# Performance work log

Measured on AMD Instinct MI355X. Metric: run time of the kernel, lower is better.

Reference implementation:

```python
import jax, jax.numpy as jnp
import numpy as np

A, B = 0.0, 1.0
U_LEFT, U_RIGHT = 0.0, 0.0
BOUNDARY_PENALTY = 10.0
N_POINTS = 32768
K_TEST = 1024  # sine test functions
LAYERS = [1, 256, 256, 256, 1]


def setup_inputs() -> dict:
    key = jax.random.key(0)
    ks = jax.random.split(key, 2 + len(LAYERS) - 1)
    # Gauss-Lobatto-like nodes: sorted points in (A, B)
    x = jnp.sort(jax.random.uniform(ks[0], (N_POINTS, 1), dtype=jnp.float32,
                                    minval=A, maxval=B), axis=0)
    # positive quadrature weights, scaled so sum(weights) ~ (B - A)
    weights = jax.random.uniform(ks[1], (N_POINTS,), dtype=jnp.float32) * (2.0 * (B - A) / N_POINTS)
    inp = {"x": x, "weights": weights}
    for i in range(len(LAYERS) - 1):
        fin, fout = LAYERS[i], LAYERS[i + 1]
        inp[f"W{i}"] = jax.random.normal(ks[2 + i], (fin, fout), dtype=jnp.float32) / np.sqrt(fin).astype(np.float32)
        inp[f"b{i}"] = jnp.zeros((fout,), dtype=jnp.float32)
    return inp


def _mlp(h, params):
    # tanh MLP, no activation on the last layer (matches MLP.forward)
    n = len(params)
    for i, (W, b) in enumerate(params):
        h = h @ W + b
        if i < n - 1:
            h = jnp.tanh(h)
    return h


def reference(x, weights, W0, b0, W1, b1, W2, b2, W3, b3):
    params = [(W0, b0), (W1, b1), (W2, b2), (W3, b3)]
    xf = x[:, 0]                                   # [N]

    u = _mlp(x, params)                            # [N, 1]

    # u_xx at every quadrature node via grad-of-grad, vmapped over points
    def u_scalar(xv):
        return _mlp(xv.reshape(1, 1), params)[0, 0]
    u_xx = jax.vmap(jax.grad(jax.grad(u_scalar)))(xf)   # [N]

    # analytic sine test functions v_k(x) = sin(pi k x), k = 1..K
    k = jnp.arange(1, K_TEST + 1, dtype=x.dtype)        # [K]
    test = jnp.sin(jnp.pi * k[:, None] * xf[None, :])   # [K, N]

    source = jnp.sin(jnp.pi * xf)                       # f(x) on the grid, [N]

    # batched quadrature: one matvec replaces the per-k Integrate loop
    Fk = test @ (weights * source)                      # [K]
    Rk = -(test @ (weights * u_xx))                     # [K]  (method 1: -int u_xx v_k)

    loss_interior = jnp.mean((Rk - Fk) ** 2)
    loss_boundary = 0.5 * BOUNDARY_PENALTY * (
        (u[0, 0] - U_LEFT) ** 2 + (u[-1, 0] - U_RIGHT) ** 2
    )
    return jnp.stack([loss_interior, loss_boundary])
```

## Files before the change

kernel.cpp:

```cpp
#include <hip/hip_runtime.h>
#include <cmath>

#define N_PTS 32768
#define HID   256
#define KTEST 1024
#define MB    32
#define RS    264
#define SKC   256
#define SKYB  (N_PTS / SKC)
#define SKGRID (4 * SKYB)

typedef float  f32x4  __attribute__((ext_vector_type(4)));
typedef short  s16x8  __attribute__((ext_vector_type(8)));
typedef __bf16 bf16x8 __attribute__((ext_vector_type(8)));

__device__ __forceinline__ float b2f(unsigned short s) {
    return __uint_as_float(((unsigned int)s) << 16);
}
__device__ __forceinline__ unsigned short cvt16(float x) {
    return __builtin_bit_cast(unsigned short, (__bf16)x);
}
__device__ __forceinline__ void split2(float x, unsigned short& hi, unsigned short& lo) {
    unsigned int b = __float_as_uint(x);
    hi = (unsigned short)(b >> 16);
    float hf = __uint_as_float(b & 0xFFFF0000u);
    lo = cvt16(x - hf);
}
__device__ __forceinline__ float fast_tanh(float z) {
    float e = __expf(2.0f * z);
    return 1.0f - 2.0f / (e + 1.0f);
}

__global__ __launch_bounds__(64) void wswz_kernel(
    const float* __restrict__ W1, const float* __restrict__ W2,
    unsigned short* __restrict__ Wh1, unsigned short* __restrict__ Wl1,
    unsigned short* __restrict__ Wh2, unsigned short* __restrict__ Wl2,
    unsigned int* __restrict__ counter)
{
    const int lane = threadIdx.x;
    const int t  = blockIdx.x;
    const int kc = blockIdx.y;
    const float* W = blockIdx.z ? W2 : W1;
    unsigned short* Wh = blockIdx.z ? Wh2 : Wh1;
    unsigned short* Wl = blockIdx.z ? Wl2 : Wl1;
    const int q = lane >> 4, ln = lane & 15;
    const int n = t * 16 + ln;
    const int kbase = kc * 32 + q * 8;

    s16x8 hv, lv;
    #pragma unroll
    for (int j = 0; j < 8; ++j) {
        unsigned short h, l;
        split2(W[(kbase + j) * HID + n], h, l);
        hv[j] = (short)h; lv[j] = (short)l;
    }
    const int out = ((t * 8 + kc) * 64 + lane) * 8;
    *(s16x8*)(Wh + out) = hv;
    *(s16x8*)(Wl + out) = lv;

    if (lane == 0 && t == 0 && kc == 0 && blockIdx.z == 0)
        *counter = 0u;
}

__global__ __launch_bounds__(512, 4) void mlp_kernel(
    const float* __restrict__ x, const float* __restrict__ wq,
    const float* __restrict__ W0, const float* __restrict__ b0,
    const float* __restrict__ b1v, const float* __restrict__ b2v,
    const float* __restrict__ W3, const float* __restrict__ b3,
    const unsigned short* __restrict__ W1h, const unsigned short* __restrict__ W1l,
    const unsigned short* __restrict__ W2h, const unsigned short* __restrict__ W2l,
    float* __restrict__ u_arr, float* __restrict__ d_arr)
{
    __shared__ __align__(16) unsigned short Hb[3][MB][RS];

    const int tid = threadIdx.x;
    const int gp0 = blockIdx.x * MB;

    {
        const int m = tid & 31, jseg = tid >> 5;
        const float xm = x[gp0 + m];
        #pragma unroll 4
        for (int jj = 0; jj < 16; ++jj) {
            int j = jseg * 16 + jj;
            float w = W0[j];
            float z = fmaf(xm, w, b0[j]);
            float y = fast_tanh(z);
            float s = 1.0f - y * y;
            float yp = s * w;
            float ypp = -2.0f * y * yp * w;
            Hb[0][m][j] = cvt16(y);
            Hb[1][m][j] = cvt16(yp);
            Hb[2][m][j] = cvt16(ypp);
        }
    }
    __syncthreads();

    const int lane = tid & 63, wv = tid >> 6;
    const int q = lane >> 4, ln = lane & 15;

    const int fragbase = (wv * 2) * 8 * 512 + lane * 8;

    for (int layer = 0; layer < 2; ++layer) {
        const unsigned short* __restrict__ WhW = (layer ? W2h : W1h) + fragbase;
        const unsigned short* __restrict__ WlW = (layer ? W2l : W1l) + fragbase;
        const float* __restrict__ bb = layer ? b2v : b1v;

        f32x4 acc[3][2][2];
        #pragma unroll
        for (int s = 0; s < 3; ++s)
            #pragma unroll
            for (int mf = 0; mf < 2; ++mf)
                #pragma unroll
                for (int nt = 0; nt < 2; ++nt)
                    acc[s][mf][nt] = (f32x4){0.f, 0.f, 0.f, 0.f};

        s16x8 bh[2][2], bl[2][2];
        #pragma unroll
        for (int nt = 0; nt < 2; ++nt) {
            bh[0][nt] = *(const s16x8*)(WhW + nt * 4096);
            bl[0][nt] = *(const s16x8*)(WlW + nt * 4096);
        }

        int cur = 0;
        for (int kc = 0; kc < 8; ++kc) {
            const int nxt = cur ^ 1;
            if (kc < 7) {
                #pragma unroll
                for (int nt = 0; nt < 2; ++nt) {
                    const int off = nt * 4096 + (kc + 1) * 512;
                    bh[nxt][nt] = *(const s16x8*)(WhW + off);
                    bl[nxt][nt] = *(const s16x8*)(WlW + off);
                }
            }
            s16x8 av[3][2];
            #pragma unroll
            for (int s = 0; s < 3; ++s)
                #pragma unroll
                for (int mf = 0; mf < 2; ++mf)
                    av[s][mf] = *(const s16x8*)&Hb[s][mf * 16 + ln][kc * 32 + q * 8];
            #pragma unroll
            for (int s = 0; s < 3; ++s)
                #pragma unroll
                for (int mf = 0; mf < 2; ++mf)
                    #pragma unroll
                    for (int nt = 0; nt < 2; ++nt) {
                        acc[s][mf][nt] = __builtin_amdgcn_mfma_f32_16x16x32_bf16(
                            __builtin_bit_cast(bf16x8, av[s][mf]),
                            __builtin_bit_cast(bf16x8, bh[cur][nt]), acc[s][mf][nt], 0, 0, 0);
                        acc[s][mf][nt] = __builtin_amdgcn_mfma_f32_16x16x32_bf16(
                            __builtin_bit_cast(bf16x8, av[s][mf]),
                            __builtin_bit_cast(bf16x8, bl[cur][nt]), acc[s][mf][nt], 0, 0, 0);
                    }
            cur = nxt;
        }
        __syncthreads();

        #pragma unroll
        for (int nt = 0; nt < 2; ++nt) {
            const int c = wv * 32 + nt * 16 + ln;
            const float bias = bb[c];
            #pragma unroll
            for (int mf = 0; mf < 2; ++mf) {
                #pragma unroll
                for (int i = 0; i < 4; ++i) {
                    const int r = mf * 16 + q * 4 + i;
                    float z   = acc[0][mf][nt][i] + bias;
                    float zp  = acc[1][mf][nt][i];
                    float zpp = acc[2][mf][nt][i];
                    float y  = fast_tanh(z);
                    float s  = 1.0f - y * y;
                    float yp = s * zp;
                    float ypp = fmaf(s, zpp, -2.0f * y * yp * zp);
                    Hb[0][r][c] = cvt16(y);
                    if (layer == 0) Hb[1][r][c] = cvt16(yp);
                    Hb[2][r][c] = cvt16(ypp);
                }
            }
        }
        __syncthreads();
    }

    float* psum = (float*)&Hb[1][0][0];
    {
        const int m = tid & 31, seg = tid >> 5;
        float su = 0.f, sx = 0.f;
        #pragma unroll 4
        for (int jj = 0; jj < 16; ++jj) {
            int j = seg * 16 + jj;
            float w3 = W3[j];
            su = fmaf(b2f(Hb[0][m][j]), w3, su);
            sx = fmaf(b2f(Hb[2][m][j]), w3, sx);
        }
        psum[(0 * 16 + seg) * 32 + m] = su;
        psum[(1 * 16 + seg) * 32 + m] = sx;
    }
    __syncthreads();
    if (tid < MB) {
        float u = b3[0], uxx = 0.f;
        #pragma unroll
        for (int s2 = 0; s2 < 16; ++s2) {
            u   += psum[s2 * 32 + tid];
            uxx += psum[(16 + s2) * 32 + tid];
        }
        const int gp = gp0 + tid;
        u_arr[gp] = u;
        float xv = x[gp];
        d_arr[gp] = -wq[gp] * (uxx + sinpif(xv));
    }
}

__global__ __launch_bounds__(256) void sk_loss_kernel(
    const float* __restrict__ x, const float* __restrict__ d_arr,
    const float* __restrict__ u_arr, float* __restrict__ part,
    unsigned int* __restrict__ counter, float* __restrict__ out)
{
    __shared__ float xs_h[SKC], xs_l[SKC], ds[SKC];
    __shared__ float red[4];
    __shared__ int lastFlag;

    const int tid = threadIdx.x;
    const int k = blockIdx.x * 256 + tid;
    const int i0 = blockIdx.y * SKC;

    {
        float xv = x[i0 + tid];
        float xh = __uint_as_float(__float_as_uint(xv) & 0xFFFFF000u);
        xs_h[tid] = xh * 0.5f;
        xs_l[tid] = (xv - xh) * 0.5f;
        ds[tid]   = d_arr[i0 + tid];
    }
    __syncthreads();

    const float kf = (float)(k + 1);
    float s = 0.f;
    #pragma unroll 8
    for (int i = 0; i < SKC; ++i) {
        float A = kf * xs_h[i];
        float f = __builtin_amdgcn_fractf(A);
        float t = __builtin_amdgcn_fractf(fmaf(kf, xs_l[i], f));
        s = fmaf(__builtin_amdgcn_sinf(t), ds[i], s);
    }
    part[blockIdx.y * KTEST + k] = s;

    __threadfence();
    if (tid == 0)
        lastFlag = (atomicAdd(counter, 1u) == (unsigned)(SKGRID - 1));
    __syncthreads();
    if (!lastFlag) return;
    __threadfence();

    float a0 = 0.f, a1 = 0.f, a2 = 0.f, a3 = 0.f;
    const float* P = part + tid * 4;
    for (int yb = 0; yb < SKYB; ++yb) {
        f32x4 v = *(const f32x4*)(P + yb * KTEST);
        a0 += v[0]; a1 += v[1]; a2 += v[2]; a3 += v[3];
    }
    float sq = a0 * a0 + a1 * a1 + a2 * a2 + a3 * a3;
    #pragma unroll
    for (int off = 32; off > 0; off >>= 1) sq += __shfl_down(sq, off, 64);
    if ((tid & 63) == 0) red[tid >> 6] = sq;
    __syncthreads();
    if (tid == 0) {
        float t = red[0] + red[1] + red[2] + red[3];
        out[0] = t * (1.0f / (float)KTEST);
        float u0 = u_arr[0], uN = u_arr[N_PTS - 1];
        out[1] = 5.0f * (u0 * u0 + uN * uN);
    }
}

extern "C" void kernel_launch(void* const* d_in, const int* in_sizes, int n_in,
                              void* d_out, int out_size, void* d_ws, size_t ws_size,
                              hipStream_t stream)
{
    const float* x  = (const float*)d_in[0];
    const float* wq = (const float*)d_in[1];
    const float* W0 = (const float*)d_in[2];
    const float* b0 = (const float*)d_in[3];
    const float* W1 = (const float*)d_in[4];
    const float* b1 = (const float*)d_in[5];
    const float* W2 = (const float*)d_in[6];
    const float* b2 = (const float*)d_in[7];
    const float* W3 = (const float*)d_in[8];
    const float* b3 = (const float*)d_in[9];
    float* out = (float*)d_out;

    float* ws    = (float*)d_ws;
    float* u_arr = ws;
    float* d_arr = ws + N_PTS;
    float* part  = ws + 2 * N_PTS;
    unsigned short* W1h = (unsigned short*)(ws + 2 * N_PTS + SKYB * KTEST);
    unsigned short* W1l = W1h + HID * HID;
    unsigned short* W2h = W1l + HID * HID;
    unsigned short* W2l = W2h + HID * HID;
    unsigned int* counter = (unsigned int*)(W2l + HID * HID);

    wswz_kernel<<<dim3(16, 8, 2), 64, 0, stream>>>(W1, W2, W1h, W1l, W2h, W2l, counter);
    mlp_kernel<<<N_PTS / MB, 512, 0, stream>>>(x, wq, W0, b0, b1, b2, W3, b3,
                                               W1h, W1l, W2h, W2l, u_arr, d_arr);
    sk_loss_kernel<<<dim3(4, SKYB), 256, 0, stream>>>(x, d_arr, u_arr, part, counter, out);
}
```

Baseline: 161.8 us.

## Fuse sine quadrature into MLP kernel and switch to 32x32 MFMA tiles

Removes the separate quadrature kernel. Each MLP block now computes its 32 points' contribution to all 1024 sine test sums and atomically adds them into one of 8 replicated accumulators. The last block reduces these into the loss. The MFMA tiling also changes from 16x16x32 to 32x32x16, with the weight swizzle and epilogue row mapping updated to match. This removes the d_arr/u_arr round trip and a kernel launch, at the cost of heavy atomic traffic (1024 atomics per block across 1024 blocks) and a duplicated final reduction block that looks like leftover code.

```diff
diff --git a/kernel.cpp b/kernel.cpp
--- a/kernel.cpp
+++ b/kernel.cpp
@@ -6,13 +6,12 @@
 #define KTEST 1024
 #define MB    32
 #define RS    264
-#define SKC   256
-#define SKYB  (N_PTS / SKC)
-#define SKGRID (4 * SKYB)
-
-typedef float  f32x4  __attribute__((ext_vector_type(4)));
-typedef short  s16x8  __attribute__((ext_vector_type(8)));
-typedef __bf16 bf16x8 __attribute__((ext_vector_type(8)));
+#define NREP  8
+
+typedef float  f32x4   __attribute__((ext_vector_type(4)));
+typedef float  f32x16  __attribute__((ext_vector_type(16)));
+typedef short  s16x8   __attribute__((ext_vector_type(8)));
+typedef __bf16 bf16x8  __attribute__((ext_vector_type(8)));
 
 __device__ __forceinline__ float b2f(unsigned short s) {
     return __uint_as_float(((unsigned int)s) << 16);
@@ -35,7 +34,7 @@
     const float* __restrict__ W1, const float* __restrict__ W2,
     unsigned short* __restrict__ Wh1, unsigned short* __restrict__ Wl1,
     unsigned short* __restrict__ Wh2, unsigned short* __restrict__ Wl2,
-    unsigned int* __restrict__ counter)
+    float* __restrict__ SkRep, unsigned int* __restrict__ counter)
 {
     const int lane = threadIdx.x;
     const int t  = blockIdx.x;
@@ -43,9 +42,9 @@
     const float* W = blockIdx.z ? W2 : W1;
     unsigned short* Wh = blockIdx.z ? Wh2 : Wh1;
     unsigned short* Wl = blockIdx.z ? Wl2 : Wl1;
-    const int q = lane >> 4, ln = lane & 15;
-    const int n = t * 16 + ln;
-    const int kbase = kc * 32 + q * 8;
+    const int half = lane >> 5, ln = lane & 31;
+    const int n = t * 32 + ln;
+    const int kbase = kc * 16 + half * 8;
 
     s16x8 hv, lv;
     #pragma unroll
@@ -54,11 +53,13 @@
         split2(W[(kbase + j) * HID + n], h, l);
         hv[j] = (short)h; lv[j] = (short)l;
     }
-    const int out = ((t * 8 + kc) * 64 + lane) * 8;
+    const int out = ((t * 16 + kc) * 64 + lane) * 8;
     *(s16x8*)(Wh + out) = hv;
     *(s16x8*)(Wl + out) = lv;
 
-    if (lane == 0 && t == 0 && kc == 0 && blockIdx.z == 0)
+    if (blockIdx.z == 0)
+        SkRep[(t * 16 + kc) * 64 + lane] = 0.f;
+    if (lane == 0 && t == 0 && kc == 0 && blockIdx.z == 1)
         *counter = 0u;
 }
 
@@ -69,9 +70,12 @@
     const float* __restrict__ W3, const float* __restrict__ b3,
     const unsigned short* __restrict__ W1h, const unsigned short* __restrict__ W1l,
     const unsigned short* __restrict__ W2h, const unsigned short* __restrict__ W2l,
-    float* __restrict__ u_arr, float* __restrict__ d_arr)
+    float* __restrict__ u_bnd, float* __restrict__ SkRep,
+    unsigned int* __restrict__ counter, float* __restrict__ out)
 {
     __shared__ __align__(16) unsigned short Hb[3][MB][RS];
+    __shared__ float red[4];
+    __shared__ int lastFlag;
 
     const int tid = threadIdx.x;
     const int gp0 = blockIdx.x * MB;
@@ -96,86 +100,59 @@
     __syncthreads();
 
     const int lane = tid & 63, wv = tid >> 6;
-    const int q = lane >> 4, ln = lane & 15;
-
-    const int fragbase = (wv * 2) * 8 * 512 + lane * 8;
+    const int half = lane >> 5, ln = lane & 31;
+
+    const int fragbase = (wv * 16) * 512 + lane * 8;
 
     for (int layer = 0; layer < 2; ++layer) {
         const unsigned short* __restrict__ WhW = (layer ? W2h : W1h) + fragbase;
         const unsigned short* __restrict__ WlW = (layer ? W2l : W1l) + fragbase;
         const float* __restrict__ bb = layer ? b2v : b1v;
 
-        f32x4 acc[3][2][2];
-        #pragma unroll
-        for (int s = 0; s < 3; ++s)
+        f32x16 acc[3];
+        #pragma unroll
+        for (int s = 0; s < 3; ++s) acc[s] = (f32x16)(0.f);
+
+        s16x8 bh[2], bl[2];
+        bh[0] = *(const s16x8*)(WhW);
+        bl[0] = *(const s16x8*)(WlW);
+
+        int cur = 0;
+        for (int kc = 0; kc < 16; ++kc) {
+            const int nxt = cur ^ 1;
+            if (kc < 15) {
+                bh[nxt] = *(const s16x8*)(WhW + (kc + 1) * 512);
+                bl[nxt] = *(const s16x8*)(WlW + (kc + 1) * 512);
+            }
             #pragma unroll
-            for (int mf = 0; mf < 2; ++mf)
-                #pragma unroll
-                for (int nt = 0; nt < 2; ++nt)
-                    acc[s][mf][nt] = (f32x4){0.f, 0.f, 0.f, 0.f};
-
-        s16x8 bh[2][2], bl[2][2];
-        #pragma unroll
-        for (int nt = 0; nt < 2; ++nt) {
-            bh[0][nt] = *(const s16x8*)(WhW + nt * 4096);
-            bl[0][nt] = *(const s16x8*)(WlW + nt * 4096);
-        }
-
-        int cur = 0;
-        for (int kc = 0; kc < 8; ++kc) {
-            const int nxt = cur ^ 1;
-            if (kc < 7) {
-                #pragma unroll
-                for (int nt = 0; nt < 2; ++nt) {
-                    const int off = nt * 4096 + (kc + 1) * 512;
-                    bh[nxt][nt] = *(const s16x8*)(WhW + off);
-                    bl[nxt][nt] = *(const s16x8*)(WlW + off);
-                }
+            for (int s = 0; s < 3; ++s) {
+                s16x8 av = *(const s16x8*)&Hb[s][ln][kc * 16 + half * 8];
+                acc[s] = __builtin_amdgcn_mfma_f32_32x32x16_bf16(
+                    __builtin_bit_cast(bf16x8, av),
+                    __builtin_bit_cast(bf16x8, bh[cur]), acc[s], 0, 0, 0);
+                acc[s] = __builtin_amdgcn_mfma_f32_32x32x16_bf16(
+                    __builtin_bit_cast(bf16x8, av),
+                    __builtin_bit_cast(bf16x8, bl[cur]), acc[s], 0, 0, 0);
             }
-            s16x8 av[3][2];
-            #pragma unroll
-            for (int s = 0; s < 3; ++s)
-                #pragma unroll
-                for (int mf = 0; mf < 2; ++mf)
-                    av[s][mf] = *(const s16x8*)&Hb[s][mf * 16 + ln][kc * 32 + q * 8];
-            #pragma unroll
-            for (int s = 0; s < 3; ++s)
-                #pragma unroll
-                for (int mf = 0; mf < 2; ++mf)
-                    #pragma unroll
-                    for (int nt = 0; nt < 2; ++nt) {
-                        acc[s][mf][nt] = __builtin_amdgcn_mfma_f32_16x16x32_bf16(
-                            __builtin_bit_cast(bf16x8, av[s][mf]),
-                            __builtin_bit_cast(bf16x8, bh[cur][nt]), acc[s][mf][nt], 0, 0, 0);
-                        acc[s][mf][nt] = __builtin_amdgcn_mfma_f32_16x16x32_bf16(
-                            __builtin_bit_cast(bf16x8, av[s][mf]),
-                            __builtin_bit_cast(bf16x8, bl[cur][nt]), acc[s][mf][nt], 0, 0, 0);
-                    }
             cur = nxt;
         }
         __syncthreads();
 
-        #pragma unroll
-        for (int nt = 0; nt < 2; ++nt) {
-            const int c = wv * 32 + nt * 16 + ln;
-            const float bias = bb[c];
-            #pragma unroll
-            for (int mf = 0; mf < 2; ++mf) {
-                #pragma unroll
-                for (int i = 0; i < 4; ++i) {
-                    const int r = mf * 16 + q * 4 + i;
-                    float z   = acc[0][mf][nt][i] + bias;
-                    float zp  = acc[1][mf][nt][i];
-                    float zpp = acc[2][mf][nt][i];
-                    float y  = fast_tanh(z);
-                    float s  = 1.0f - y * y;
-                    float yp = s * zp;
-                    float ypp = fmaf(s, zpp, -2.0f * y * yp * zp);
-                    Hb[0][r][c] = cvt16(y);
-                    if (layer == 0) Hb[1][r][c] = cvt16(yp);
-                    Hb[2][r][c] = cvt16(ypp);
-                }
-            }
+        const int c = wv * 32 + ln;
+        const float bias = bb[c];
+        #pragma unroll
+        for (int r = 0; r < 16; ++r) {
+            const int row = (r & 3) + 8 * (r >> 2) + 4 * half;
+            float z   = acc[0][r] + bias;
+            float zp  = acc[1][r];
+            float zpp = acc[2][r];
+            float y  = fast_tanh(z);
+            float s  = 1.0f - y * y;
+            float yp = s * zp;
+            float ypp = fmaf(s, zpp, -2.0f * y * yp * zp);
+            Hb[0][row][c] = cvt16(y);
+            if (layer == 0) Hb[1][row][c] = cvt16(yp);
+            Hb[2][row][c] = cvt16(ypp);
         }
         __syncthreads();
     }
@@ -195,6 +172,8 @@
         psum[(1 * 16 + seg) * 32 + m] = sx;
     }
     __syncthreads();
+
+    float* aux = (float*)&Hb[2][0][0];
     if (tid < MB) {
         float u = b3[0], uxx = 0.f;
         #pragma unroll
@@ -203,68 +182,87 @@
             uxx += psum[(16 + s2) * 32 + tid];
         }
         const int gp = gp0 + tid;
-        u_arr[gp] = u;
         float xv = x[gp];
-        d_arr[gp] = -wq[gp] * (uxx + sinpif(xv));
-    }
-}
-
-__global__ __launch_bounds__(256) void sk_loss_kernel(
-    const float* __restrict__ x, const float* __restrict__ d_arr,
-    const float* __restrict__ u_arr, float* __restrict__ part,
-    unsigned int* __restrict__ counter, float* __restrict__ out)
-{
-    __shared__ float xs_h[SKC], xs_l[SKC], ds[SKC];
-    __shared__ float red[4];
-    __shared__ int lastFlag;
-
-    const int tid = threadIdx.x;
-    const int k = blockIdx.x * 256 + tid;
-    const int i0 = blockIdx.y * SKC;
-
-    {
-        float xv = x[i0 + tid];
+        aux[tid] = -wq[gp] * (uxx + __builtin_amdgcn_sinf(0.5f * xv));
         float xh = __uint_as_float(__float_as_uint(xv) & 0xFFFFF000u);
-        xs_h[tid] = xh * 0.5f;
-        xs_l[tid] = (xv - xh) * 0.5f;
-        ds[tid]   = d_arr[i0 + tid];
-    }
-    __syncthreads();
-
-    const float kf = (float)(k + 1);
-    float s = 0.f;
-    #pragma unroll 8
-    for (int i = 0; i < SKC; ++i) {
-        float A = kf * xs_h[i];
-        float f = __builtin_amdgcn_fractf(A);
-        float t = __builtin_amdgcn_fractf(fmaf(kf, xs_l[i], f));
-        s = fmaf(__builtin_amdgcn_sinf(t), ds[i], s);
-    }
-    part[blockIdx.y * KTEST + k] = s;
+        aux[32 + tid] = xh * 0.5f;
+        aux[64 + tid] = (xv - xh) * 0.5f;
+        if (gp == 0)          u_bnd[0] = u;
+        if (gp == N_PTS - 1)  u_bnd[1] = u;
+    }
+    __syncthreads();
+
+    {
+        const float kf1 = (float)(tid + 1);
+        const float kf2 = (float)(tid + 513);
+        float s1 = 0.f, s2 = 0.f;
+        #pragma unroll 8
+        for (int i = 0; i < MB; ++i) {
+            float dv = aux[i], xh2 = aux[32 + i], xl2 = aux[64 + i];
+            float A1 = kf1 * xh2;
+            float f1 = __builtin_amdgcn_fractf(A1);
+            float t1 = __builtin_amdgcn_fractf(fmaf(kf1, xl2, f1));
+            s1 = fmaf(__builtin_amdgcn_sinf(t1), dv, s1);
+            float A2 = kf2 * xh2;
+            float f2 = __builtin_amdgcn_fractf(A2);
+            float t2 = __builtin_amdgcn_fractf(fmaf(kf2, xl2, f2));
+            s2 = fmaf(__builtin_amdgcn_sinf(t2), dv, s2);
+        }
+        float* rep = SkRep + (blockIdx.x & (NREP - 1)) * KTEST;
+        atomicAdd(rep + tid, s1);
+        atomicAdd(rep + tid + 512, s2);
+    }
 
     __threadfence();
     if (tid == 0)
-        lastFlag = (atomicAdd(counter, 1u) == (unsigned)(SKGRID - 1));
+        lastFlag = (atomicAdd(counter, 1u) == (unsigned)(gridDim.x - 1));
     __syncthreads();
     if (!lastFlag) return;
     __threadfence();
 
-    float a0 = 0.f, a1 = 0.f, a2 = 0.f, a3 = 0.f;
-    const float* P = part + tid * 4;
-    for (int yb = 0; yb < SKYB; ++yb) {
-        f32x4 v = *(const f32x4*)(P + yb * KTEST);
-        a0 += v[0]; a1 += v[1]; a2 += v[2]; a3 += v[3];
-    }
-    float sq = a0 * a0 + a1 * a1 + a2 * a2 + a3 * a3;
-    #pragma unroll
-    for (int off = 32; off > 0; off >>= 1) sq += __shfl_down(sq, off, 64);
-    if ((tid & 63) == 0) red[tid >> 6] = sq;
-    __syncthreads();
-    if (tid == 0) {
-        float t = red[0] + red[1] + red[2] + red[3];
-        out[0] = t * (1.0f / (float)KTEST);
-        float u0 = u_arr[0], uN = u_arr[N_PTS - 1];
-        out[1] = 5.0f * (u0 * u0 + uN * uN);
+    {
+        const volatile float* SR = SkRep;
+        float a1 = 0.f, a2 = 0.f;
+        #pragma unroll
+        for (int r = 0; r < NREP; ++r) {
+            a1 += SR[r * KTEST + tid];
+            a2 += SR[r * KTEST + tid + 512];
+        }
+        float sq = a1 * a1 + a2 * a2;
+        #pragma unroll
+        for (int off = 32; off > 0; off >>= 1) sq += __shfl_down(sq, off, 64);
+        if ((tid & 63) == 0) red[tid >> 6] = sq;
+        __syncthreads();
+        if (tid == 0) {
+            float t = red[0] + red[1] + red[2] + red[3] +
+                      red[0] * 0.f;
+            out[0] = t;
+        }
+        __syncthreads();
+    }
+    {
+        float* aux = (float*)&Hb[2][0][0];
+        const volatile float* SR = SkRep;
+        float a1 = 0.f, a2 = 0.f;
+        #pragma unroll
+        for (int r = 0; r < NREP; ++r) {
+            a1 += SR[r * KTEST + tid];
+            a2 += SR[r * KTEST + tid + 512];
+        }
+        float sq = a1 * a1 + a2 * a2;
+        #pragma unroll
+        for (int off = 32; off > 0; off >>= 1) sq += __shfl_down(sq, off, 64);
+        if ((tid & 63) == 0) aux[tid >> 6] = sq;
+        __syncthreads();
+        if (tid == 0) {
+            float t = 0.f;
+            #pragma unroll
+            for (int w = 0; w < 8; ++w) t += aux[w];
+            out[0] = t * (1.0f / (float)KTEST);
+            const volatile float* ub = u_bnd;
+            float u0 = ub[0], uN = ub[1];
+            out[1] = 5.0f * (u0 * u0 + uN * uN);
+        }
     }
 }
 
@@ -284,18 +282,18 @@
     const float* b3 = (const float*)d_in[9];
     float* out = (float*)d_out;
 
-    float* ws    = (float*)d_ws;
-    float* u_arr = ws;
-    float* d_arr = ws + N_PTS;
-    float* part  = ws + 2 * N_PTS;
-    unsigned short* W1h = (unsigned short*)(ws + 2 * N_PTS + SKYB * KTEST);
+    float* ws     = (float*)d_ws;
+    float* u_bnd  = ws;
+    float* SkRep  = ws + 4;
+    unsigned short* W1h = (unsigned short*)(ws + 4 + NREP * KTEST);
     unsigned short* W1l = W1h + HID * HID;
     unsigned short* W2h = W1l + HID * HID;
     unsigned short* W2l = W2h + HID * HID;
     unsigned int* counter = (unsigned int*)(W2l + HID * HID);
 
-    wswz_kernel<<<dim3(16, 8, 2), 64, 0, stream>>>(W1, W2, W1h, W1l, W2h, W2l, counter);
+    wswz_kernel<<<dim3(8, 16, 2), 64, 0, stream>>>(W1, W2, W1h, W1l, W2h, W2l,
+                                                   SkRep, counter);
     mlp_kernel<<<N_PTS / MB, 512, 0, stream>>>(x, wq, W0, b0, b1, b2, W3, b3,
-                                               W1h, W1l, W2h, W2l, u_arr, d_arr);
-    sk_loss_kernel<<<dim3(4, SKYB), 256, 0, stream>>>(x, d_arr, u_arr, part, counter, out);
-}
+                                               W1h, W1l, W2h, W2l,
+                                               u_bnd, SkRep, counter, out);
+}
```

Measured after the change: 250.5 us. +54.8%, slower.
